# Optimization experiments

Measured on AMD Instinct MI355X. Metric: run time of the kernel, lower is better.

Reference implementation:

```python
import jax, jax.numpy as jnp
import numpy as np

N_NODES = 50000
N_EDGES = 800000
F_IN = 24
H = 128
N_GRAPHS = 100
BN_EPS = 1e-5


def setup_inputs() -> dict:
    key = jax.random.key(0)
    ks = jax.random.split(key, 12)
    x = jax.random.normal(ks[0], (N_NODES, F_IN), dtype=jnp.float32)
    edge_index = jax.random.randint(ks[1], (2, N_EDGES), 0, N_NODES, dtype=jnp.int32)
    batch = (jnp.arange(N_NODES, dtype=jnp.int32) // (N_NODES // N_GRAPHS)).astype(jnp.int32)

    def lin(k, fan_in, fan_out):
        bound = 1.0 / np.sqrt(fan_in)
        kw, kb = jax.random.split(k)
        W = jax.random.uniform(kw, (fan_in, fan_out), jnp.float32, -bound, bound)
        b = jax.random.uniform(kb, (fan_out,), jnp.float32, -bound, bound)
        return W, b

    W1, b1 = lin(ks[2], 2 * F_IN, H)
    W2, b2 = lin(ks[3], 2 * H, H)
    W3, b3 = lin(ks[4], 2 * H, H)
    Wl, bl = lin(ks[5], H, 1)
    g1 = jnp.ones((H,), jnp.float32); be1 = jnp.zeros((H,), jnp.float32)
    g2 = jnp.ones((H,), jnp.float32); be2 = jnp.zeros((H,), jnp.float32)
    g3 = jnp.ones((H,), jnp.float32); be3 = jnp.zeros((H,), jnp.float32)
    return {"x": x, "edge_index": edge_index, "batch": batch,
            "W1": W1, "b1": b1, "W2": W2, "b2": b2, "W3": W3, "b3": b3,
            "g1": g1, "be1": be1, "g2": g2, "be2": be2, "g3": g3, "be3": be3,
            "Wl": Wl, "bl": bl}


def edge_conv(x, src, dst, W, b):
    # PyG EdgeConv: message = mlp([x_i, x_j - x_i]) for edge j->i, aggr=max at i
    x_i = x[dst]                                    # [E, F]
    e = jnp.concatenate([x_i, x[src] - x_i], axis=-1)  # [E, 2F]
    m = jax.nn.relu(e @ W + b)                      # [E, H]
    out = jax.ops.segment_max(m, dst, num_segments=N_NODES)
    return jnp.where(jnp.isfinite(out), out, 0.0)   # isolated nodes -> 0


def batch_norm(h, g, b):
    # training-mode BN over node dim (biased variance), dropout treated as identity
    mu = h.mean(axis=0)
    var = ((h - mu) ** 2).mean(axis=0)
    return g * (h - mu) * jax.lax.rsqrt(var + BN_EPS) + b


def reference(x, edge_index, batch, W1, b1, W2, b2, W3, b3,
              g1, be1, g2, be2, g3, be3, Wl, bl):
    src, dst = edge_index[0], edge_index[1]
    h = edge_conv(x, src, dst, W1, b1)
    h = jax.nn.relu(batch_norm(h, g1, be1))
    h = edge_conv(h, src, dst, W2, b2)
    h = jax.nn.relu(batch_norm(h, g2, be2))
    h = edge_conv(h, src, dst, W3, b3)
    h = batch_norm(h, g3, be3)
    # global_mean_pool
    sums = jax.ops.segment_sum(h, batch, num_segments=N_GRAPHS)           # [G, H]
    counts = jax.ops.segment_sum(jnp.ones((h.shape[0],), h.dtype), batch,
                                 num_segments=N_GRAPHS)
    pooled = sums / jnp.maximum(counts, 1.0)[:, None]
    return jax.nn.relu(pooled @ Wl + bl)                                  # [G, 1]
```

## Files before the change

kernel.cpp:

```cpp
#include <hip/hip_runtime.h>

#define N_NODES 50000
#define N_EDGES 800000
#define F_IN 24
#define HDIM 128
#define N_GRAPHS 100
#define BN_EPS 1e-5f
#define NBLK 196
#define ROWS_PER_GRAPH (N_NODES / N_GRAPHS)
#define MM_GRID 782
#define HIST_BLKS ((N_EDGES + 255) / 256)
#define PREP_BLKS (F_IN + 2 * HDIM)
#define SSTR 32
#define SUMS_PER_LAYER (256 * SSTR)
#define STATS_BLKS 196

typedef _Float16 h2 __attribute__((ext_vector_type(2)));
typedef _Float16 h4 __attribute__((ext_vector_type(4)));
typedef _Float16 f16x8 __attribute__((ext_vector_type(8)));
typedef float f32x4 __attribute__((ext_vector_type(4)));

template <int K, int KC>
__global__ __launch_bounds__(256) void k_mm1(const float* __restrict__ X,
                                             const float* __restrict__ Wcat,
                                             const float* __restrict__ bias,
                                             float* __restrict__ A, _Float16* __restrict__ C) {
    __shared__ float Xs[KC * 68];
    __shared__ float Ws[KC * 128];
    int tid = threadIdx.x;
    int row0 = blockIdx.x * 64;
    const bool isA = (blockIdx.y == 0);
    const int colbase = isA ? 0 : 128;
    int cg = tid & 31;
    int rg = tid >> 5;

    float acc[8][4];
#pragma unroll
    for (int ri = 0; ri < 8; ++ri)
#pragma unroll
        for (int ci = 0; ci < 4; ++ci)
            acc[ri][ci] = isA ? bias[cg * 4 + ci] : 0.f;

    for (int k0 = 0; k0 < K; k0 += KC) {
        __syncthreads();
        {
            const int C4 = KC / 4;
            for (int i = tid; i < 64 * C4; i += 256) {
                int c4 = i % C4, r = i / C4;
                int row = row0 + r;
                float4 v = make_float4(0.f, 0.f, 0.f, 0.f);
                if (row < N_NODES) v = *(const float4*)&X[row * K + k0 + c4 * 4];
                Xs[(c4 * 4 + 0) * 68 + r] = v.x;
                Xs[(c4 * 4 + 1) * 68 + r] = v.y;
                Xs[(c4 * 4 + 2) * 68 + r] = v.z;
                Xs[(c4 * 4 + 3) * 68 + r] = v.w;
            }
        }
        for (int i = tid; i < KC * 32; i += 256) {
            int c4 = i & 31, kr = i >> 5;
            *(float4*)&Ws[kr * 128 + c4 * 4] =
                *(const float4*)&Wcat[(k0 + kr) * 256 + colbase + c4 * 4];
        }
        __syncthreads();
#pragma unroll
        for (int kk = 0; kk < KC; ++kk) {
            float4 t0 = *(const float4*)&Xs[kk * 68 + rg * 8];
            float4 t1 = *(const float4*)&Xs[kk * 68 + rg * 8 + 4];
            float4 w = *(const float4*)&Ws[kk * 128 + cg * 4];
            float t[8] = {t0.x, t0.y, t0.z, t0.w, t1.x, t1.y, t1.z, t1.w};
            float wv[4] = {w.x, w.y, w.z, w.w};
#pragma unroll
            for (int ri = 0; ri < 8; ++ri)
#pragma unroll
                for (int ci = 0; ci < 4; ++ci)
                    acc[ri][ci] += t[ri] * wv[ci];
        }
    }

#pragma unroll
    for (int ri = 0; ri < 8; ++ri) {
        int row = row0 + rg * 8 + ri;
        if (row < N_NODES) {
            if (isA) {
                *(float4*)&A[row * HDIM + cg * 4] =
                    make_float4(acc[ri][0], acc[ri][1], acc[ri][2], acc[ri][3]);
            } else {
                union { h2 h[2]; uint2 u; } pk;
                pk.h[0] = h2{(_Float16)acc[ri][0], (_Float16)acc[ri][1]};
                pk.h[1] = h2{(_Float16)acc[ri][2], (_Float16)acc[ri][3]};
                *(uint2*)&C[row * HDIM + cg * 4] = pk.u;
            }
        }
    }
}

__global__ __launch_bounds__(256) void k_mmf(const _Float16* __restrict__ X,
                                             const _Float16* __restrict__ Wf,
                                             const float* __restrict__ bias,
                                             const float* __restrict__ sums,
                                             const float* __restrict__ g,
                                             const float* __restrict__ be,
                                             float* __restrict__ A, _Float16* __restrict__ C) {
    __shared__ _Float16 Xh[16 * 520];
    __shared__ _Float16 Wh[128 * 128];
    __shared__ float scs[128], shs[128];
    int tid = threadIdx.x;
    int lane = tid & 63, wv = tid >> 6;
    int row0 = blockIdx.x * 64;
    const bool isA = (blockIdx.y == 0);
    const _Float16* Wsrc = Wf + (isA ? 0 : 16384);

    if (tid < 128) {
        float S  = sums[tid * SSTR];
        float S2 = sums[(128 + tid) * SSTR];
        float mean = S / (float)N_NODES;
        float var = fmaxf(S2 / (float)N_NODES - mean * mean, 0.f);
        float scv = g[tid] / sqrtf(var + BN_EPS);
        scs[tid] = scv;
        shs[tid] = be[tid] - mean * scv;
    }
    {
        const uint4* s = (const uint4*)Wsrc;
        uint4* d = (uint4*)Wh;
        for (int i = tid; i < 2048; i += 256) d[i] = s[i];
    }
    __syncthreads();
    for (int i = tid; i < 64 * 32; i += 256) {
        int k4 = i & 31, rl = i >> 5;
        int row = row0 + rl;
        float4 v = make_float4(0.f, 0.f, 0.f, 0.f);
        if (row < N_NODES) {
            h4 xv = *(const h4*)&X[row * HDIM + k4 * 4];
            v = make_float4((float)xv.x, (float)xv.y, (float)xv.z, (float)xv.w);
        }
        int c = k4 * 4;
        v.x = fmaxf(v.x * scs[c + 0] + shs[c + 0], 0.f);
        v.y = fmaxf(v.y * scs[c + 1] + shs[c + 1], 0.f);
        v.z = fmaxf(v.z * scs[c + 2] + shs[c + 2], 0.f);
        v.w = fmaxf(v.w * scs[c + 3] + shs[c + 3], 0.f);
        int rt = rl >> 4, m = rl & 15, kc = k4 >> 3, q = (k4 >> 1) & 3, jh = k4 & 1;
        _Float16* d = Xh + (rt * 4 + kc) * 520 + (q * 16 + m) * 8 + jh * 4;
        d[0] = (_Float16)v.x; d[1] = (_Float16)v.y;
        d[2] = (_Float16)v.z; d[3] = (_Float16)v.w;
    }
    __syncthreads();

    int n = lane & 15, q = lane >> 4;
    f32x4 acc[8];
#pragma unroll
    for (int nt = 0; nt < 8; ++nt) {
        float b0 = isA ? bias[nt * 16 + n] : 0.f;
        acc[nt] = f32x4{b0, b0, b0, b0};
    }
#pragma unroll
    for (int kc = 0; kc < 4; ++kc) {
        f16x8 a = *(const f16x8*)(Xh + (wv * 4 + kc) * 520 + lane * 8);
#pragma unroll
        for (int nt = 0; nt < 8; ++nt) {
            f16x8 b = *(const f16x8*)(Wh + ((nt * 4 + kc) * 64 + lane) * 8);
            acc[nt] = __builtin_amdgcn_mfma_f32_16x16x32_f16(a, b, acc[nt], 0, 0, 0);
        }
    }
#pragma unroll
    for (int nt = 0; nt < 8; ++nt) {
#pragma unroll
        for (int r = 0; r < 4; ++r) {
            int row = row0 + wv * 16 + q * 4 + r;
            if (row < N_NODES) {
                int col = nt * 16 + n;
                if (isA) A[row * HDIM + col] = acc[nt][r];
                else     C[row * HDIM + col] = (_Float16)acc[nt][r];
            }
        }
    }
}

__global__ void k_pre(const float* __restrict__ W1, const float* __restrict__ W2,
                      const float* __restrict__ W3, float* __restrict__ Wcat1,
                      _Float16* __restrict__ Wf2, _Float16* __restrict__ Wf3,
                      const int* __restrict__ dst, unsigned* __restrict__ deg,
                      unsigned* __restrict__ rank) {
    int b = blockIdx.x;
    int j = threadIdx.x;
    if (b < F_IN) {
        float wb = W1[(b + F_IN) * HDIM + (j & 127)];
        float wt = W1[b * HDIM + (j & 127)];
        Wcat1[b * 256 + j] = (j < HDIM) ? (wt - wb) : wb;
    } else if (b < PREP_BLKS) {
        int idx = b - F_IN;
        int layer = idx >> 7;
        int k = idx & 127;
        const float* W = layer ? W3 : W2;
        _Float16* Wf   = layer ? Wf3 : Wf2;
        int col = j & 127;
        float wt = W[k * HDIM + col];
        float wb = W[(k + HDIM) * HDIM + col];
        float v = (j < 128) ? (wt - wb) : wb;
        int plane = j >> 7;
        int nt = col >> 4, n = col & 15, kc = k >> 5, q = (k >> 3) & 3, jj = k & 7;
        int f = ((nt * 4 + kc) * 4 + q) * 128 + n * 8 + jj;
        Wf[plane * 16384 + f] = (_Float16)v;
    } else {
        int e = (b - PREP_BLKS) * 256 + j;
        if (e < N_EDGES) rank[e] = atomicAdd(&deg[dst[e]], 1u);
    }
}

__global__ __launch_bounds__(256) void k_scanall(const unsigned* __restrict__ deg,
                                                 unsigned* __restrict__ bsum,
                                                 unsigned* __restrict__ off) {
    __shared__ unsigned s[256];
    int t = threadIdx.x;
    int b = blockIdx.x;
    int i = b * 256 + t;
    unsigned v = (i < N_NODES) ? deg[i] : 0u;
    s[t] = v;
    __syncthreads();
    for (int d = 1; d < 256; d <<= 1) {
        unsigned u = (t >= d) ? s[t - d] : 0u;
        __syncthreads();
        s[t] += u;
        __syncthreads();
    }
    unsigned locex = s[t] - v;
    if (t == 255) atomicExch(&bsum[b], s[255] + 1u);
    __syncthreads();
    unsigned bs = 0;
    if (t < NBLK) {
        unsigned x;
        do { x = atomicAdd(&bsum[t], 0u); } while (x == 0u);
        bs = x - 1u;
    }
    s[t] = (t < NBLK) ? bs : 0u;
    __syncthreads();
    for (int d = 1; d < 256; d <<= 1) {
        unsigned u = (t >= d) ? s[t - d] : 0u;
        __syncthreads();
        s[t] += u;
        __syncthreads();
    }
    unsigned bexcl = (b == 0) ? 0u : s[b - 1];
    if (i < N_NODES) off[i] = bexcl + locex;
}

__global__ void k_scatter(const int* __restrict__ src, const int* __restrict__ dst,
                          const unsigned* __restrict__ off, const unsigned* __restrict__ rank,
                          unsigned* __restrict__ ssrc) {
    int e = blockIdx.x * 256 + threadIdx.x;
    if (e < N_EDGES)
        ssrc[off[dst[e]] + rank[e]] = (unsigned)src[e];
}

__global__ __launch_bounds__(256) void k_agg(const float* __restrict__ A,
                                             const h2* __restrict__ Cc,
                                             const unsigned* __restrict__ off,
                                             const unsigned* __restrict__ deg,
                                             const unsigned* __restrict__ ssrc,
                                             h2* __restrict__ H) {
    __shared__ unsigned sl[4][64];
    int w = threadIdx.x >> 6;
    int lane = threadIdx.x & 63;
    int i = blockIdx.x * 4 + w;
    int d = (int)deg[i];
    unsigned o = off[i];
    union { unsigned short us[2]; h2 v; } ninf;
    ninf.us[0] = 0xFC00; ninf.us[1] = 0xFC00;
    h2 m2 = ninf.v;
    for (int base = 0; base < d; base += 64) {
        int cntc = min(64, d - base);
        if (lane < cntc) sl[w][lane] = ssrc[o + base + lane];
        int e = 0;
        for (; e + 8 <= cntc; e += 8) {
            unsigned s0 = sl[w][e + 0], s1 = sl[w][e + 1], s2 = sl[w][e + 2], s3 = sl[w][e + 3];
            unsigned s4 = sl[w][e + 4], s5 = sl[w][e + 5], s6 = sl[w][e + 6], s7 = sl[w][e + 7];
            h2 v0 = Cc[s0 * 64 + lane];
            h2 v1 = Cc[s1 * 64 + lane];
            h2 v2 = Cc[s2 * 64 + lane];
            h2 v3 = Cc[s3 * 64 + lane];
            h2 v4 = Cc[s4 * 64 + lane];
            h2 v5 = Cc[s5 * 64 + lane];
            h2 v6 = Cc[s6 * 64 + lane];
            h2 v7 = Cc[s7 * 64 + lane];
            h2 a0 = __builtin_elementwise_max(v0, v1);
            h2 a1 = __builtin_elementwise_max(v2, v3);
            h2 a2 = __builtin_elementwise_max(v4, v5);
            h2 a3 = __builtin_elementwise_max(v6, v7);
            h2 b0 = __builtin_elementwise_max(a0, a1);
            h2 b1 = __builtin_elementwise_max(a2, a3);
            m2 = __builtin_elementwise_max(m2, __builtin_elementwise_max(b0, b1));
        }
        if (e + 4 <= cntc) {
            unsigned s0 = sl[w][e + 0], s1 = sl[w][e + 1], s2 = sl[w][e + 2], s3 = sl[w][e + 3];
            h2 v0 = Cc[s0 * 64 + lane];
            h2 v1 = Cc[s1 * 64 + lane];
            h2 v2 = Cc[s2 * 64 + lane];
            h2 v3 = Cc[s3 * 64 + lane];
            h2 a0 = __builtin_elementwise_max(v0, v1);
            h2 a1 = __builtin_elementwise_max(v2, v3);
            m2 = __builtin_elementwise_max(m2, __builtin_elementwise_max(a0, a1));
            e += 4;
        }
        for (; e < cntc; ++e)
            m2 = __builtin_elementwise_max(m2, Cc[sl[w][e] * 64 + lane]);
    }
    float2 a = *(const float2*)&A[i * HDIM + lane * 2];
    float hx = (d > 0) ? fmaxf(a.x + (float)m2.x, 0.f) : 0.f;
    float hy = (d > 0) ? fmaxf(a.y + (float)m2.y, 0.f) : 0.f;
    H[i * 64 + lane] = h2{(_Float16)hx, (_Float16)hy};
}

__global__ __launch_bounds__(256) void k_stats(const _Float16* __restrict__ H,
                                               float* __restrict__ sums) {
    __shared__ float4 ls[256], ls2[256];
    int t = threadIdx.x;
    int c4 = t & 31, rg = t >> 5;
    int row0 = blockIdx.x * 256;
    float4 s = make_float4(0.f, 0.f, 0.f, 0.f);
    float4 s2 = make_float4(0.f, 0.f, 0.f, 0.f);
#pragma unroll 4
    for (int it = 0; it < 32; ++it) {
        int row = row0 + rg * 32 + it;
        if (row < N_NODES) {
            h4 hv = *(const h4*)&H[row * HDIM + c4 * 4];
            float4 v = make_float4((float)hv.x, (float)hv.y, (float)hv.z, (float)hv.w);
            s.x += v.x; s.y += v.y; s.z += v.z; s.w += v.w;
            s2.x += v.x * v.x; s2.y += v.y * v.y; s2.z += v.z * v.z; s2.w += v.w * v.w;
        }
    }
    ls[t] = s; ls2[t] = s2;
    __syncthreads();
    if (t < 32) {
        float4 a = ls[t], a2 = ls2[t];
#pragma unroll
        for (int j = 1; j < 8; ++j) {
            float4 b = ls[j * 32 + t], b2 = ls2[j * 32 + t];
            a.x += b.x; a.y += b.y; a.z += b.z; a.w += b.w;
            a2.x += b2.x; a2.y += b2.y; a2.z += b2.z; a2.w += b2.w;
        }
        int c = t * 4;
        atomicAdd(&sums[(c + 0) * SSTR], a.x);
        atomicAdd(&sums[(c + 1) * SSTR], a.y);
        atomicAdd(&sums[(c + 2) * SSTR], a.z);
        atomicAdd(&sums[(c + 3) * SSTR], a.w);
        atomicAdd(&sums[(128 + c + 0) * SSTR], a2.x);
        atomicAdd(&sums[(128 + c + 1) * SSTR], a2.y);
        atomicAdd(&sums[(128 + c + 2) * SSTR], a2.z);
        atomicAdd(&sums[(128 + c + 3) * SSTR], a2.w);
    }
}

__global__ __launch_bounds__(128) void k_poolsum(const _Float16* __restrict__ H,
                                                 float* __restrict__ Pg,
                                                 float* __restrict__ sums) {
    int g = blockIdx.x;
    int k = threadIdx.x;
    const _Float16* base = H + (size_t)g * ROWS_PER_GRAPH * HDIM;
    float s = 0.f, s2 = 0.f;
#pragma unroll 4
    for (int r = 0; r < ROWS_PER_GRAPH; ++r) {
        float v = (float)base[r * HDIM + k];
        s += v; s2 += v * v;
    }
    Pg[g * HDIM + k] = s;
    atomicAdd(&sums[k * SSTR], s);
    atomicAdd(&sums[(128 + k) * SSTR], s2);
}

__global__ __launch_bounds__(128) void k_out(const float* __restrict__ Pg,
                                             const float* __restrict__ sums,
                                             const float* __restrict__ g3,
                                             const float* __restrict__ be3,
                                             const float* __restrict__ Wl,
                                             const float* __restrict__ bl,
                                             float* __restrict__ out) {
    int g = blockIdx.x;
    int k = threadIdx.x;
    float S  = sums[k * SSTR];
    float S2 = sums[(128 + k) * SSTR];
    float mean = S / (float)N_NODES;
    float var = fmaxf(S2 / (float)N_NODES - mean * mean, 0.f);
    float scv = g3[k] / sqrtf(var + BN_EPS);
    float shv = be3[k] - mean * scv;
    float p = (scv * (Pg[g * HDIM + k] * (1.f / (float)ROWS_PER_GRAPH)) + shv) * Wl[k];
    __shared__ float red[2];
    for (int o = 32; o > 0; o >>= 1) p += __shfl_down(p, o);
    if ((k & 63) == 0) red[k >> 6] = p;
    __syncthreads();
    if (k == 0) out[g] = fmaxf(red[0] + red[1] + bl[0], 0.f);
}

extern "C" void kernel_launch(void* const* d_in, const int* in_sizes, int n_in,
                              void* d_out, int out_size, void* d_ws, size_t ws_size,
                              hipStream_t stream) {
    const float* x   = (const float*)d_in[0];
    const int* ei    = (const int*)d_in[1];
    const float* W1  = (const float*)d_in[3];
    const float* b1  = (const float*)d_in[4];
    const float* W2  = (const float*)d_in[5];
    const float* b2  = (const float*)d_in[6];
    const float* W3  = (const float*)d_in[7];
    const float* b3  = (const float*)d_in[8];
    const float* g1  = (const float*)d_in[9];
    const float* be1 = (const float*)d_in[10];
    const float* g2  = (const float*)d_in[11];
    const float* be2 = (const float*)d_in[12];
    const float* g3  = (const float*)d_in[13];
    const float* be3 = (const float*)d_in[14];
    const float* Wl  = (const float*)d_in[15];
    const float* bl  = (const float*)d_in[16];
    float* out = (float*)d_out;

    const int* srcp = ei;
    const int* dstp = ei + N_EDGES;

    char* ws = (char*)d_ws;
    size_t o = 0;
    auto alloc = [&](size_t bytes) -> void* {
        o = (o + 255) & ~(size_t)255;
        void* p = ws + o;
        o += bytes;
        return p;
    };
    float* A      = (float*)alloc((size_t)N_NODES * HDIM * 4);
    _Float16* C   = (_Float16*)alloc((size_t)N_NODES * HDIM * 2);
    _Float16* h   = (_Float16*)alloc((size_t)N_NODES * HDIM * 2);
    float* Wcat1  = (float*)alloc((size_t)F_IN * 256 * 4);
    _Float16* Wf2 = (_Float16*)alloc((size_t)2 * 16384 * 2);
    _Float16* Wf3 = (_Float16*)alloc((size_t)2 * 16384 * 2);
    unsigned* deg  = (unsigned*)alloc((size_t)N_NODES * 4);
    unsigned* bsum = (unsigned*)alloc((size_t)NBLK * 4);
    float* sums    = (float*)alloc((size_t)3 * SUMS_PER_LAYER * 4);
    unsigned* off  = (unsigned*)alloc((size_t)N_NODES * 4);
    unsigned* rank = (unsigned*)alloc((size_t)N_EDGES * 4);
    unsigned* ssrc = (unsigned*)alloc((size_t)N_EDGES * 4);
    float* Pg      = (float*)alloc((size_t)N_GRAPHS * HDIM * 4);
    (void)ws_size; (void)n_in; (void)in_sizes; (void)out_size;

    float* sums0 = sums;
    float* sums1 = sums + SUMS_PER_LAYER;
    float* sums2 = sums + 2 * SUMS_PER_LAYER;

    size_t zlen = (size_t)((char*)(sums + 3 * SUMS_PER_LAYER) - (char*)deg);
    (void)hipMemsetAsync(deg, 0, zlen, stream);

    k_pre<<<PREP_BLKS + HIST_BLKS, 256, 0, stream>>>(W1, W2, W3, Wcat1, Wf2, Wf3,
                                                     dstp, deg, rank);
    k_scanall<<<NBLK, 256, 0, stream>>>(deg, bsum, off);
    k_scatter<<<HIST_BLKS, 256, 0, stream>>>(srcp, dstp, off, rank, ssrc);

    const dim3 MMG(MM_GRID, 2);
    const int AGB = N_NODES / 4;

    k_mm1<F_IN, F_IN><<<MMG, 256, 0, stream>>>(x, Wcat1, b1, A, C);
    k_agg<<<AGB, 256, 0, stream>>>(A, (const h2*)C, off, deg, ssrc, (h2*)h);
    k_stats<<<STATS_BLKS, 256, 0, stream>>>(h, sums0);

    k_mmf<<<MMG, 256, 0, stream>>>(h, Wf2, b2, sums0, g1, be1, A, C);
    k_agg<<<AGB, 256, 0, stream>>>(A, (const h2*)C, off, deg, ssrc, (h2*)h);
    k_stats<<<STATS_BLKS, 256, 0, stream>>>(h, sums1);

    k_mmf<<<MMG, 256, 0, stream>>>(h, Wf3, b3, sums1, g2, be2, A, C);
    k_agg<<<AGB, 256, 0, stream>>>(A, (const h2*)C, off, deg, ssrc, (h2*)h);

    k_poolsum<<<N_GRAPHS, 128, 0, stream>>>(h, Pg, sums2);
    k_out<<<N_GRAPHS, 128, 0, stream>>>(Pg, sums2, g3, be3, Wl, bl, out);
}
```

Measured before the change: 400.4 us.

## Parallelize final pooling, halve stats rows per block, add nontemporal hints

The final pool kernel goes from 100 blocks of 128 threads, each walking 500 rows, to 1000 blocks of 256 threads that each reduce a 50-row chunk. The chunk partial sums are then added up in k_out. The stats kernel now uses twice as many blocks with half the rows each. Nontemporal loads and stores are added for A, H and ssrc to cut cache pollution. The cost is more atomics on the per-channel sums and an extra partial-sum buffer, and the nontemporal hints may hurt if the data would otherwise stay in L2 for the next kernel.

```diff
diff --git a/kernel.cpp b/kernel.cpp
--- a/kernel.cpp
+++ b/kernel.cpp
@@ -13,12 +13,16 @@
 #define PREP_BLKS (F_IN + 2 * HDIM)
 #define SSTR 32
 #define SUMS_PER_LAYER (256 * SSTR)
-#define STATS_BLKS 196
+#define STATS_BLKS 392
+#define POOL_CHUNKS 10
+#define POOL_BLKS (N_GRAPHS * POOL_CHUNKS)
+#define ROWS_PER_CHUNK (ROWS_PER_GRAPH / POOL_CHUNKS)
 
 typedef _Float16 h2 __attribute__((ext_vector_type(2)));
 typedef _Float16 h4 __attribute__((ext_vector_type(4)));
 typedef _Float16 f16x8 __attribute__((ext_vector_type(8)));
 typedef float f32x4 __attribute__((ext_vector_type(4)));
+typedef float f32x2 __attribute__((ext_vector_type(2)));
 
 template <int K, int KC>
 __global__ __launch_bounds__(256) void k_mm1(const float* __restrict__ X,
@@ -82,8 +86,8 @@
         int row = row0 + rg * 8 + ri;
         if (row < N_NODES) {
             if (isA) {
-                *(float4*)&A[row * HDIM + cg * 4] =
-                    make_float4(acc[ri][0], acc[ri][1], acc[ri][2], acc[ri][3]);
+                f32x4 av = {acc[ri][0], acc[ri][1], acc[ri][2], acc[ri][3]};
+                __builtin_nontemporal_store(av, (f32x4*)&A[row * HDIM + cg * 4]);
             } else {
                 union { h2 h[2]; uint2 u; } pk;
                 pk.h[0] = h2{(_Float16)acc[ri][0], (_Float16)acc[ri][1]};
@@ -168,7 +172,7 @@
             int row = row0 + wv * 16 + q * 4 + r;
             if (row < N_NODES) {
                 int col = nt * 16 + n;
-                if (isA) A[row * HDIM + col] = acc[nt][r];
+                if (isA) __builtin_nontemporal_store(acc[nt][r], &A[row * HDIM + col]);
                 else     C[row * HDIM + col] = (_Float16)acc[nt][r];
             }
         }
@@ -268,7 +272,7 @@
     h2 m2 = ninf.v;
     for (int base = 0; base < d; base += 64) {
         int cntc = min(64, d - base);
-        if (lane < cntc) sl[w][lane] = ssrc[o + base + lane];
+        if (lane < cntc) sl[w][lane] = __builtin_nontemporal_load(&ssrc[o + base + lane]);
         int e = 0;
         for (; e + 8 <= cntc; e += 8) {
             unsigned s0 = sl[w][e + 0], s1 = sl[w][e + 1], s2 = sl[w][e + 2], s3 = sl[w][e + 3];
@@ -303,10 +307,10 @@
         for (; e < cntc; ++e)
             m2 = __builtin_elementwise_max(m2, Cc[sl[w][e] * 64 + lane]);
     }
-    float2 a = *(const float2*)&A[i * HDIM + lane * 2];
+    f32x2 a = __builtin_nontemporal_load((const f32x2*)&A[i * HDIM + lane * 2]);
     float hx = (d > 0) ? fmaxf(a.x + (float)m2.x, 0.f) : 0.f;
     float hy = (d > 0) ? fmaxf(a.y + (float)m2.y, 0.f) : 0.f;
-    H[i * 64 + lane] = h2{(_Float16)hx, (_Float16)hy};
+    __builtin_nontemporal_store(h2{(_Float16)hx, (_Float16)hy}, &H[i * 64 + lane]);
 }
 
 __global__ __launch_bounds__(256) void k_stats(const _Float16* __restrict__ H,
@@ -314,12 +318,12 @@
     __shared__ float4 ls[256], ls2[256];
     int t = threadIdx.x;
     int c4 = t & 31, rg = t >> 5;
-    int row0 = blockIdx.x * 256;
+    int row0 = blockIdx.x * 128;
     float4 s = make_float4(0.f, 0.f, 0.f, 0.f);
     float4 s2 = make_float4(0.f, 0.f, 0.f, 0.f);
 #pragma unroll 4
-    for (int it = 0; it < 32; ++it) {
-        int row = row0 + rg * 32 + it;
+    for (int it = 0; it < 16; ++it) {
+        int row = row0 + rg * 16 + it;
         if (row < N_NODES) {
             h4 hv = *(const h4*)&H[row * HDIM + c4 * 4];
             float4 v = make_float4((float)hv.x, (float)hv.y, (float)hv.z, (float)hv.w);
@@ -349,24 +353,51 @@
     }
 }
 
-__global__ __launch_bounds__(128) void k_poolsum(const _Float16* __restrict__ H,
-                                                 float* __restrict__ Pg,
-                                                 float* __restrict__ sums) {
-    int g = blockIdx.x;
-    int k = threadIdx.x;
-    const _Float16* base = H + (size_t)g * ROWS_PER_GRAPH * HDIM;
-    float s = 0.f, s2 = 0.f;
-#pragma unroll 4
-    for (int r = 0; r < ROWS_PER_GRAPH; ++r) {
-        float v = (float)base[r * HDIM + k];
-        s += v; s2 += v * v;
-    }
-    Pg[g * HDIM + k] = s;
-    atomicAdd(&sums[k * SSTR], s);
-    atomicAdd(&sums[(128 + k) * SSTR], s2);
-}
-
-__global__ __launch_bounds__(128) void k_out(const float* __restrict__ Pg,
+__global__ __launch_bounds__(256) void k_pool2(const _Float16* __restrict__ H,
+                                               float* __restrict__ Pp,
+                                               float* __restrict__ sums) {
+    __shared__ float4 ls[256], ls2[256];
+    int t = threadIdx.x;
+    int c4 = t & 31, rg = t >> 5;
+    int b = blockIdx.x;
+    int base = (b / POOL_CHUNKS) * ROWS_PER_GRAPH + (b % POOL_CHUNKS) * ROWS_PER_CHUNK;
+    float4 s = make_float4(0.f, 0.f, 0.f, 0.f);
+    float4 s2 = make_float4(0.f, 0.f, 0.f, 0.f);
+#pragma unroll
+    for (int j = 0; j < 7; ++j) {
+        int rl = rg + j * 8;
+        if (rl < ROWS_PER_CHUNK) {
+            int row = base + rl;
+            h4 hv = __builtin_nontemporal_load((const h4*)&H[row * HDIM + c4 * 4]);
+            float4 v = make_float4((float)hv.x, (float)hv.y, (float)hv.z, (float)hv.w);
+            s.x += v.x; s.y += v.y; s.z += v.z; s.w += v.w;
+            s2.x += v.x * v.x; s2.y += v.y * v.y; s2.z += v.z * v.z; s2.w += v.w * v.w;
+        }
+    }
+    ls[t] = s; ls2[t] = s2;
+    __syncthreads();
+    if (t < 32) {
+        float4 a = ls[t], a2 = ls2[t];
+#pragma unroll
+        for (int j = 1; j < 8; ++j) {
+            float4 q = ls[j * 32 + t], q2 = ls2[j * 32 + t];
+            a.x += q.x; a.y += q.y; a.z += q.z; a.w += q.w;
+            a2.x += q2.x; a2.y += q2.y; a2.z += q2.z; a2.w += q2.w;
+        }
+        int c = t * 4;
+        *(float4*)&Pp[b * HDIM + c] = a;
+        atomicAdd(&sums[(c + 0) * SSTR], a.x);
+        atomicAdd(&sums[(c + 1) * SSTR], a.y);
+        atomicAdd(&sums[(c + 2) * SSTR], a.z);
+        atomicAdd(&sums[(c + 3) * SSTR], a.w);
+        atomicAdd(&sums[(128 + c + 0) * SSTR], a2.x);
+        atomicAdd(&sums[(128 + c + 1) * SSTR], a2.y);
+        atomicAdd(&sums[(128 + c + 2) * SSTR], a2.z);
+        atomicAdd(&sums[(128 + c + 3) * SSTR], a2.w);
+    }
+}
+
+__global__ __launch_bounds__(128) void k_out(const float* __restrict__ Pp,
                                              const float* __restrict__ sums,
                                              const float* __restrict__ g3,
                                              const float* __restrict__ be3,
@@ -381,7 +412,11 @@
     float var = fmaxf(S2 / (float)N_NODES - mean * mean, 0.f);
     float scv = g3[k] / sqrtf(var + BN_EPS);
     float shv = be3[k] - mean * scv;
-    float p = (scv * (Pg[g * HDIM + k] * (1.f / (float)ROWS_PER_GRAPH)) + shv) * Wl[k];
+    float pooled = 0.f;
+#pragma unroll
+    for (int j = 0; j < POOL_CHUNKS; ++j)
+        pooled += Pp[(g * POOL_CHUNKS + j) * HDIM + k];
+    float p = (scv * (pooled * (1.f / (float)ROWS_PER_GRAPH)) + shv) * Wl[k];
     __shared__ float red[2];
     for (int o = 32; o > 0; o >>= 1) p += __shfl_down(p, o);
     if ((k & 63) == 0) red[k >> 6] = p;
@@ -433,7 +468,7 @@
     unsigned* off  = (unsigned*)alloc((size_t)N_NODES * 4);
     unsigned* rank = (unsigned*)alloc((size_t)N_EDGES * 4);
     unsigned* ssrc = (unsigned*)alloc((size_t)N_EDGES * 4);
-    float* Pg      = (float*)alloc((size_t)N_GRAPHS * HDIM * 4);
+    float* Pp      = (float*)alloc((size_t)POOL_BLKS * HDIM * 4);
     (void)ws_size; (void)n_in; (void)in_sizes; (void)out_size;
 
     float* sums0 = sums;
@@ -462,6 +497,6 @@
     k_mmf<<<MMG, 256, 0, stream>>>(h, Wf3, b3, sums1, g2, be2, A, C);
     k_agg<<<AGB, 256, 0, stream>>>(A, (const h2*)C, off, deg, ssrc, (h2*)h);
 
-    k_poolsum<<<N_GRAPHS, 128, 0, stream>>>(h, Pg, sums2);
-    k_out<<<N_GRAPHS, 128, 0, stream>>>(Pg, sums2, g3, be3, Wl, bl, out);
-}
+    k_pool2<<<POOL_BLKS, 256, 0, stream>>>(h, Pp, sums2);
+    k_out<<<N_GRAPHS, 128, 0, stream>>>(Pp, sums2, g3, be3, Wl, bl, out);
+}
```

After: 404.6 us. No clear change (+1.0%).
